# Kernel optimization log

Hardware: AMD Instinct MI355X
Metric: run time of the kernel (lower is better)

The kernel has to match this reference:

```python
import jax, jax.numpy as jnp
import numpy as np

EPS = 1e-8  # torch cosine_similarity default eps


def setup_inputs() -> dict:
    key = jax.random.key(0)
    k1, k2, k3 = jax.random.split(key, 3)
    B, N, D = 16, 4096, 256
    embeddings_stat = jax.random.normal(k1, (B, N, D), dtype=jnp.float32)
    embeddings_con = jax.random.normal(k2, (B, N, D), dtype=jnp.float32)
    # ragged row counts per instance (0 allowed -> instance skipped, as in source)
    lengths = jax.random.randint(k3, (B,), 0, 4096)
    return {
        "embeddings_stat": embeddings_stat,
        "embeddings_con": embeddings_con,
        "lengths": lengths,
    }


def reference(embeddings_stat, embeddings_con, lengths):
    # embeddings_stat, embeddings_con: [B, N, D]; lengths: [B] valid row counts
    B, N, D = embeddings_stat.shape
    dt = embeddings_stat.dtype
    mask = (jnp.arange(N)[None, :] < lengths[:, None]).astype(dt)  # [B, N]

    dot = jnp.sum(embeddings_stat * embeddings_con, axis=-1)        # [B, N]
    n_stat = jnp.maximum(jnp.sqrt(jnp.sum(embeddings_stat**2, -1)), EPS)
    n_con = jnp.maximum(jnp.sqrt(jnp.sum(embeddings_con**2, -1)), EPS)
    cos = dot / (n_stat * n_con)                                    # [B, N]

    denom = jnp.maximum(lengths, 1).astype(dt)                      # avoid /0
    mean_cos = jnp.sum(cos * mask, axis=-1) / denom                 # [B]
    per_inst = jnp.where(lengths > 0, 1.0 - mean_cos, 0.0)          # skip empty
    mean_cosine_loss = jnp.sum(per_inst) / B
    return mean_cosine_loss[None]  # shape [1], matching torch output
```

## Files before the change

kernel.cpp:

```cpp
#include <hip/hip_runtime.h>

#define NROWS 4096
#define DDIM  256
#define BDIM  16
#define RBLKS 256
#define BSETS 4
#define NB1 (RBLKS * BSETS)

__global__ __launch_bounds__(256) void cos_partial_kernel(
    const float* __restrict__ stat, const float* __restrict__ con,
    const int* __restrict__ lens, float* __restrict__ ws) {
  const int rblk = blockIdx.x >> 2;
  const int bset = blockIdx.x & (BSETS - 1);
  const int wave = threadIdx.x >> 6;
  const int lane = threadIdx.x & 63;
  const int g    = lane >> 4;
  const int j    = lane & 15;

  const int n  = rblk * 16 + wave * 4 + g;
  const int b0 = bset * 4;

  float acc[4];

  #pragma unroll
  for (int bi = 0; bi < 4; ++bi) {
    const int b     = b0 + bi;
    const int len   = lens[b];
    const bool valid = (n < len);

    float dot = 0.0f, ns = 0.0f, nc = 0.0f;
    if (valid) {
      const size_t base = (size_t)b * (NROWS * DDIM) + (size_t)n * DDIM + (j << 2);
      const float* pa = stat + base;
      const float* pc = con + base;
      #pragma unroll
      for (int m = 0; m < 4; ++m) {
        const float4 a = *reinterpret_cast<const float4*>(pa + (m << 6));
        const float4 c = *reinterpret_cast<const float4*>(pc + (m << 6));
        dot = fmaf(a.x, c.x, fmaf(a.y, c.y, fmaf(a.z, c.z, fmaf(a.w, c.w, dot))));
        ns  = fmaf(a.x, a.x, fmaf(a.y, a.y, fmaf(a.z, a.z, fmaf(a.w, a.w, ns))));
        nc  = fmaf(c.x, c.x, fmaf(c.y, c.y, fmaf(c.z, c.z, fmaf(c.w, c.w, nc))));
      }
    }
    #pragma unroll
    for (int off = 1; off < 16; off <<= 1) {
      dot += __shfl_xor(dot, off);
      ns  += __shfl_xor(ns,  off);
      nc  += __shfl_xor(nc,  off);
    }
    float cosv = valid ? dot * rsqrtf(ns) * rsqrtf(nc) : 0.0f;
    cosv += __shfl_xor(cosv, 16);
    cosv += __shfl_xor(cosv, 32);
    acc[bi] = cosv;
  }

  __shared__ float sh[4][4];
  if (lane == 0) {
    #pragma unroll
    for (int bi = 0; bi < 4; ++bi) sh[wave][bi] = acc[bi];
  }
  __syncthreads();
  if (threadIdx.x < 4) {
    const int b = b0 + threadIdx.x;
    ws[b * RBLKS + rblk] =
        sh[0][threadIdx.x] + sh[1][threadIdx.x] + sh[2][threadIdx.x] + sh[3][threadIdx.x];
  }
}

__global__ __launch_bounds__(256) void cos_final_kernel(
    const float* __restrict__ ws, const int* __restrict__ lens,
    float* __restrict__ out, int B) {
  const int wave = threadIdx.x >> 6;
  const int lane = threadIdx.x & 63;

  __shared__ float shl[BDIM];

  #pragma unroll
  for (int bi = 0; bi < 4; ++bi) {
    const int b = wave * 4 + bi;
    float v = 0.0f;
    #pragma unroll
    for (int m = 0; m < RBLKS / 64; ++m) v += ws[b * RBLKS + (m << 6) + lane];
    #pragma unroll
    for (int off = 1; off < 64; off <<= 1) v += __shfl_xor(v, off);
    if (lane == 0) {
      const int len = lens[b];
      shl[b] = (len > 0) ? (1.0f - v / (float)len) : 0.0f;
    }
  }
  __syncthreads();
  if (threadIdx.x == 0) {
    float t = 0.0f;
    #pragma unroll
    for (int i = 0; i < BDIM; ++i) t += shl[i];
    out[0] = t * (1.0f / BDIM);
  }
}

extern "C" void kernel_launch(void* const* d_in, const int* in_sizes, int n_in,
                              void* d_out, int out_size, void* d_ws, size_t ws_size,
                              hipStream_t stream) {
  const float* stat = (const float*)d_in[0];
  const float* con  = (const float*)d_in[1];
  const int*   lens = (const int*)d_in[2];
  float*       out  = (float*)d_out;
  float*       ws   = (float*)d_ws;

  const int B = in_sizes[2];

  dim3 grid1(NB1);
  dim3 blk1(256);
  hipLaunchKernelGGL(cos_partial_kernel, grid1, blk1, 0, stream, stat, con, lens, ws);

  dim3 grid2(1);
  dim3 blk2(256);
  hipLaunchKernelGGL(cos_final_kernel, grid2, blk2, 0, stream, ws, lens, out, B);
}
```

Before: 20.62 us.

## Fuse final reduction into partial kernel via last-block atomic counters

Merges the two-kernel reduction into one kernel. Each block publishes its partial sums and increments hierarchical group counters, and the last block to finish performs the final reduction and writes the loss. This removes the separate finalize kernel launch and its dependency gap. In exchange it adds a memset to reset the counters, plus atomic traffic on every block.

```diff
diff --git a/kernel.cpp b/kernel.cpp
--- a/kernel.cpp
+++ b/kernel.cpp
@@ -5,27 +5,30 @@
 #define BDIM  16
 #define RBLKS 256
 #define BSETS 4
-#define NB1 (RBLKS * BSETS)
+#define NB1   (RBLKS * BSETS)
+#define GRPSZ 16
+#define NGRP  (NB1 / GRPSZ)
+#define CNT_BASE 16384
+#define CNT_STRIDE 32
 
-__global__ __launch_bounds__(256) void cos_partial_kernel(
+__global__ __launch_bounds__(256) void cos_fused_kernel(
     const float* __restrict__ stat, const float* __restrict__ con,
-    const int* __restrict__ lens, float* __restrict__ ws) {
+    const int* __restrict__ lens, float* __restrict__ partial,
+    unsigned int* __restrict__ cnts, float* __restrict__ out) {
   const int rblk = blockIdx.x >> 2;
   const int bset = blockIdx.x & (BSETS - 1);
   const int wave = threadIdx.x >> 6;
   const int lane = threadIdx.x & 63;
   const int g    = lane >> 4;
   const int j    = lane & 15;
-
-  const int n  = rblk * 16 + wave * 4 + g;
-  const int b0 = bset * 4;
+  const int n    = rblk * 16 + wave * 4 + g;
+  const int b0   = bset * 4;
 
   float acc[4];
-
   #pragma unroll
   for (int bi = 0; bi < 4; ++bi) {
-    const int b     = b0 + bi;
-    const int len   = lens[b];
+    const int b      = b0 + bi;
+    const int len    = lens[b];
     const bool valid = (n < len);
 
     float dot = 0.0f, ns = 0.0f, nc = 0.0f;
@@ -55,45 +58,62 @@
   }
 
   __shared__ float sh[4][4];
+  __shared__ int   is_last;
   if (lane == 0) {
     #pragma unroll
     for (int bi = 0; bi < 4; ++bi) sh[wave][bi] = acc[bi];
   }
   __syncthreads();
-  if (threadIdx.x < 4) {
-    const int b = b0 + threadIdx.x;
-    ws[b * RBLKS + rblk] =
-        sh[0][threadIdx.x] + sh[1][threadIdx.x] + sh[2][threadIdx.x] + sh[3][threadIdx.x];
-  }
-}
 
-__global__ __launch_bounds__(256) void cos_final_kernel(
-    const float* __restrict__ ws, const int* __restrict__ lens,
-    float* __restrict__ out, int B) {
-  const int wave = threadIdx.x >> 6;
-  const int lane = threadIdx.x & 63;
-
-  __shared__ float shl[BDIM];
-
-  #pragma unroll
-  for (int bi = 0; bi < 4; ++bi) {
-    const int b = wave * 4 + bi;
-    float v = 0.0f;
+  if (threadIdx.x == 0) {
     #pragma unroll
-    for (int m = 0; m < RBLKS / 64; ++m) v += ws[b * RBLKS + (m << 6) + lane];
-    #pragma unroll
-    for (int off = 1; off < 64; off <<= 1) v += __shfl_xor(v, off);
-    if (lane == 0) {
-      const int len = lens[b];
-      shl[b] = (len > 0) ? (1.0f - v / (float)len) : 0.0f;
+    for (int bi = 0; bi < 4; ++bi) {
+      const float v = sh[0][bi] + sh[1][bi] + sh[2][bi] + sh[3][bi];
+      __hip_atomic_store(&partial[(b0 + bi) * RBLKS + rblk], v,
+                         __ATOMIC_RELAXED, __HIP_MEMORY_SCOPE_AGENT);
     }
+    int last = 0;
+    const int grp = blockIdx.x >> 4;
+    const unsigned p = __hip_atomic_fetch_add(&cnts[grp * CNT_STRIDE], 1u,
+                          __ATOMIC_RELEASE, __HIP_MEMORY_SCOPE_AGENT);
+    if (p == GRPSZ - 1) {
+      const unsigned q = __hip_atomic_fetch_add(&cnts[NGRP * CNT_STRIDE], 1u,
+                            __ATOMIC_RELEASE, __HIP_MEMORY_SCOPE_AGENT);
+      if (q == NGRP - 1) last = 1;
+    }
+    is_last = last;
   }
   __syncthreads();
-  if (threadIdx.x == 0) {
-    float t = 0.0f;
+
+  if (is_last) {
+    if (threadIdx.x == 0) {
+      (void)__hip_atomic_load(&cnts[NGRP * CNT_STRIDE], __ATOMIC_ACQUIRE,
+                              __HIP_MEMORY_SCOPE_AGENT);
+    }
+    __syncthreads();
+    __shared__ float shl[BDIM];
     #pragma unroll
-    for (int i = 0; i < BDIM; ++i) t += shl[i];
-    out[0] = t * (1.0f / BDIM);
+    for (int bi = 0; bi < 4; ++bi) {
+      const int b = wave * 4 + bi;
+      float v = 0.0f;
+      #pragma unroll
+      for (int m = 0; m < RBLKS / 64; ++m)
+        v += __hip_atomic_load(&partial[b * RBLKS + (m << 6) + lane],
+                               __ATOMIC_RELAXED, __HIP_MEMORY_SCOPE_AGENT);
+      #pragma unroll
+      for (int off = 1; off < 64; off <<= 1) v += __shfl_xor(v, off);
+      if (lane == 0) {
+        const int len = lens[b];
+        shl[b] = (len > 0) ? (1.0f - v / (float)len) : 0.0f;
+      }
+    }
+    __syncthreads();
+    if (threadIdx.x == 0) {
+      float t = 0.0f;
+      #pragma unroll
+      for (int i = 0; i < BDIM; ++i) t += shl[i];
+      out[0] = t * (1.0f / BDIM);
+    }
   }
 }
 
@@ -104,15 +124,14 @@
   const float* con  = (const float*)d_in[1];
   const int*   lens = (const int*)d_in[2];
   float*       out  = (float*)d_out;
-  float*       ws   = (float*)d_ws;
+  float*       partial = (float*)d_ws;
+  unsigned int* cnts = (unsigned int*)((char*)d_ws + CNT_BASE);
 
-  const int B = in_sizes[2];
+  hipMemsetAsync(cnts, 0, (NGRP * CNT_STRIDE + CNT_STRIDE) * sizeof(unsigned int),
+                 stream);
 
-  dim3 grid1(NB1);
-  dim3 blk1(256);
-  hipLaunchKernelGGL(cos_partial_kernel, grid1, blk1, 0, stream, stat, con, lens, ws);
-
-  dim3 grid2(1);
-  dim3 blk2(256);
-  hipLaunchKernelGGL(cos_final_kernel, grid2, blk2, 0, stream, ws, lens, out, B);
+  dim3 grid(NB1);
+  dim3 blk(256);
+  hipLaunchKernelGGL(cos_fused_kernel, grid, blk, 0, stream,
+                     stat, con, lens, partial, cnts, out);
 }
```

Result: slower. 49.79 us (+141.5%).

## Double-buffer batch loads and rotate batch-set assignment across blocks

Applied to the files above, without the earlier changes.

Each block now loads the next batch's rows into a second register set while the current batch's dot products and norms are computed, so global loads overlap arithmetic. The batch set assigned to a block is also rotated by the block-index high bits, spreading ragged batches more evenly over the grid and over time. This raises register pressure with two sets of eight float4s live, which could lower occupancy.

```diff
diff --git a/kernel.cpp b/kernel.cpp
--- a/kernel.cpp
+++ b/kernel.cpp
@@ -5,42 +5,59 @@
 #define BDIM  16
 #define RBLKS 256
 #define BSETS 4
-#define NB1 (RBLKS * BSETS)
+#define NB1   (RBLKS * BSETS)
 
 __global__ __launch_bounds__(256) void cos_partial_kernel(
     const float* __restrict__ stat, const float* __restrict__ con,
     const int* __restrict__ lens, float* __restrict__ ws) {
-  const int rblk = blockIdx.x >> 2;
-  const int bset = blockIdx.x & (BSETS - 1);
+  const int i    = blockIdx.x;
+  const int rblk = i >> 2;
+  const int bset = ((i & 3) + (i >> 8)) & 3;
   const int wave = threadIdx.x >> 6;
   const int lane = threadIdx.x & 63;
   const int g    = lane >> 4;
   const int j    = lane & 15;
+  const int n    = rblk * 16 + wave * 4 + g;
+  const int b0   = bset * 4;
 
-  const int n  = rblk * 16 + wave * 4 + g;
-  const int b0 = bset * 4;
+  const int L0 = lens[b0 + 0];
+  const int L1 = lens[b0 + 1];
+  const int L2 = lens[b0 + 2];
+  const int L3 = lens[b0 + 3];
 
-  float acc[4];
-
-  #pragma unroll
-  for (int bi = 0; bi < 4; ++bi) {
-    const int b     = b0 + bi;
-    const int len   = lens[b];
-    const bool valid = (n < len);
-
-    float dot = 0.0f, ns = 0.0f, nc = 0.0f;
-    if (valid) {
+  auto LOADS = [&](int b, int len,
+                   float4& x0, float4& x1, float4& x2, float4& x3,
+                   float4& y0, float4& y1, float4& y2, float4& y3) {
+    if (n < len) {
       const size_t base = (size_t)b * (NROWS * DDIM) + (size_t)n * DDIM + (j << 2);
       const float* pa = stat + base;
       const float* pc = con + base;
-      #pragma unroll
-      for (int m = 0; m < 4; ++m) {
-        const float4 a = *reinterpret_cast<const float4*>(pa + (m << 6));
-        const float4 c = *reinterpret_cast<const float4*>(pc + (m << 6));
-        dot = fmaf(a.x, c.x, fmaf(a.y, c.y, fmaf(a.z, c.z, fmaf(a.w, c.w, dot))));
-        ns  = fmaf(a.x, a.x, fmaf(a.y, a.y, fmaf(a.z, a.z, fmaf(a.w, a.w, ns))));
-        nc  = fmaf(c.x, c.x, fmaf(c.y, c.y, fmaf(c.z, c.z, fmaf(c.w, c.w, nc))));
-      }
+      x0 = *reinterpret_cast<const float4*>(pa);
+      x1 = *reinterpret_cast<const float4*>(pa + 64);
+      x2 = *reinterpret_cast<const float4*>(pa + 128);
+      x3 = *reinterpret_cast<const float4*>(pa + 192);
+      y0 = *reinterpret_cast<const float4*>(pc);
+      y1 = *reinterpret_cast<const float4*>(pc + 64);
+      y2 = *reinterpret_cast<const float4*>(pc + 128);
+      y3 = *reinterpret_cast<const float4*>(pc + 192);
+    } else {
+      x0 = x1 = x2 = x3 = make_float4(0.f, 0.f, 0.f, 0.f);
+      y0 = y1 = y2 = y3 = make_float4(1.f, 1.f, 1.f, 1.f);
+    }
+  };
+
+  auto COMP = [&](int len,
+                  const float4& x0, const float4& x1, const float4& x2, const float4& x3,
+                  const float4& y0, const float4& y1, const float4& y2, const float4& y3) -> float {
+    float dot = 0.f, ns = 0.f, nc = 0.f;
+    const float4 xs[4] = {x0, x1, x2, x3};
+    const float4 ys[4] = {y0, y1, y2, y3};
+    #pragma unroll
+    for (int m = 0; m < 4; ++m) {
+      const float4 a = xs[m], c = ys[m];
+      dot = fmaf(a.x, c.x, fmaf(a.y, c.y, fmaf(a.z, c.z, fmaf(a.w, c.w, dot))));
+      ns  = fmaf(a.x, a.x, fmaf(a.y, a.y, fmaf(a.z, a.z, fmaf(a.w, a.w, ns))));
+      nc  = fmaf(c.x, c.x, fmaf(c.y, c.y, fmaf(c.z, c.z, fmaf(c.w, c.w, nc))));
     }
     #pragma unroll
     for (int off = 1; off < 16; off <<= 1) {
@@ -48,16 +65,28 @@
       ns  += __shfl_xor(ns,  off);
       nc  += __shfl_xor(nc,  off);
     }
-    float cosv = valid ? dot * rsqrtf(ns) * rsqrtf(nc) : 0.0f;
+    float cosv = (n < len) ? dot * rsqrtf(ns) * rsqrtf(nc) : 0.0f;
     cosv += __shfl_xor(cosv, 16);
     cosv += __shfl_xor(cosv, 32);
-    acc[bi] = cosv;
-  }
+    return cosv;
+  };
+
+  float4 Ax0, Ax1, Ax2, Ax3, Ay0, Ay1, Ay2, Ay3;
+  float4 Bx0, Bx1, Bx2, Bx3, By0, By1, By2, By3;
+  float acc0, acc1, acc2, acc3;
+
+  LOADS(b0 + 0, L0, Ax0, Ax1, Ax2, Ax3, Ay0, Ay1, Ay2, Ay3);
+  LOADS(b0 + 1, L1, Bx0, Bx1, Bx2, Bx3, By0, By1, By2, By3);
+  acc0 = COMP(L0, Ax0, Ax1, Ax2, Ax3, Ay0, Ay1, Ay2, Ay3);
+  LOADS(b0 + 2, L2, Ax0, Ax1, Ax2, Ax3, Ay0, Ay1, Ay2, Ay3);
+  acc1 = COMP(L1, Bx0, Bx1, Bx2, Bx3, By0, By1, By2, By3);
+  LOADS(b0 + 3, L3, Bx0, Bx1, Bx2, Bx3, By0, By1, By2, By3);
+  acc2 = COMP(L2, Ax0, Ax1, Ax2, Ax3, Ay0, Ay1, Ay2, Ay3);
+  acc3 = COMP(L3, Bx0, Bx1, Bx2, Bx3, By0, By1, By2, By3);
 
   __shared__ float sh[4][4];
   if (lane == 0) {
-    #pragma unroll
-    for (int bi = 0; bi < 4; ++bi) sh[wave][bi] = acc[bi];
+    sh[wave][0] = acc0; sh[wave][1] = acc1; sh[wave][2] = acc2; sh[wave][3] = acc3;
   }
   __syncthreads();
   if (threadIdx.x < 4) {
```

Result: slower. 21.30 us (+3.3%).
